# Optimization experiments

Hardware: AMD Instinct MI355X
Metric: run time of the kernel (lower is better)

## Reference

```python
import jax, jax.numpy as jnp
import numpy as np

NUM_GROUPS = 32
EPS = 1e-5


def group_norm(x, gamma, beta):
    b, c, h, w = x.shape
    xg = x.reshape(b, NUM_GROUPS, c // NUM_GROUPS, h, w)
    mu = xg.mean(axis=(2, 3, 4), keepdims=True)
    var = xg.var(axis=(2, 3, 4), keepdims=True)
    xg = (xg - mu) * jax.lax.rsqrt(var + EPS)
    x = xg.reshape(b, c, h, w)
    return x * gamma[None, :, None, None] + beta[None, :, None, None]


def conv1x1(x, w, b):
    # 1x1 conv == per-pixel matmul over channels
    return jnp.einsum('oc,bchw->bohw', w, x) + b[None, :, None, None]


def setup_inputs() -> dict:
    key = jax.random.key(0)
    ks = jax.random.split(key, 6)
    c = 512
    scale = 0.02  # keep logits in a sane range
    return {
        'x': jax.random.normal(ks[0], (2, c, 64, 64), dtype=jnp.float32),
        'gn_w': jnp.ones((c,), jnp.float32),
        'gn_b': jnp.zeros((c,), jnp.float32),
        'wq': jax.random.normal(ks[1], (c, c), jnp.float32) * scale,
        'bq': jnp.zeros((c,), jnp.float32),
        'wk': jax.random.normal(ks[2], (c, c), jnp.float32) * scale,
        'bk': jnp.zeros((c,), jnp.float32),
        'wv': jax.random.normal(ks[3], (c, c), jnp.float32) * scale,
        'bv': jnp.zeros((c,), jnp.float32),
        'wo': jax.random.normal(ks[4], (c, c), jnp.float32) * scale,
        'bo': jnp.zeros((c,), jnp.float32),
    }


def reference(x, gn_w, gn_b, wq, bq, wk, bk, wv, bv, wo, bo):
    b, c, h, w = x.shape
    n = h * w
    h_ = group_norm(x, gn_w, gn_b)
    q = conv1x1(h_, wq, bq).reshape(b, c, n)  # (b,c,n)
    k = conv1x1(h_, wk, bk).reshape(b, c, n)
    v = conv1x1(h_, wv, bv).reshape(b, c, n)
    # scores: (b, n_q, n_k) = q^T k, scaled by c^-0.5
    scores = jnp.einsum('bcq,bck->bqk', q, k) * (c ** -0.5)
    attn = jax.nn.softmax(scores, axis=-1)
    # h_ = v @ attn^T  -> (b, c, n_q)
    out = jnp.einsum('bck,bqk->bcq', v, attn).reshape(b, c, h, w)
    return x + conv1x1(out, wo, bo)
```

## Files before the change

kernel.cpp:

```cpp
#include <hip/hip_runtime.h>

typedef __bf16 bf16_t;
typedef __bf16 bf16x8 __attribute__((ext_vector_type(8)));
typedef __bf16 bf16x4 __attribute__((ext_vector_type(4)));
typedef float  floatx4 __attribute__((ext_vector_type(4)));

#define B_  2
#define C_  512
#define N_  4096
#define EPS 1e-5f
#define SCALE 0.044194173824159216f

__device__ __forceinline__ void gl2lds16(const bf16_t* g, bf16_t* l) {
  __builtin_amdgcn_global_load_lds(
      (const __attribute__((address_space(1))) void*)g,
      (__attribute__((address_space(3))) void*)l, 16, 0, 0);
}

template <int BM, int BN>
__device__ __forceinline__ void gemm_main(
    const bf16_t* __restrict__ A, const bf16_t* __restrict__ B, int K,
    int m0, int n0, floatx4 (&acc)[BM / 32][BN / 32],
    bf16_t* __restrict__ As, bf16_t* __restrict__ Bs) {
  const int tid = threadIdx.x;
  const int w = tid >> 6, l = tid & 63;
  const int wm = (w >> 1) * (BM / 2), wn = (w & 1) * (BN / 2);
  const int lrow = l & 15, lq = l >> 4;
  const int key = lrow & 7;
  const int slot0 = lq ^ key;
  const int slot1 = (4 + lq) ^ key;

  floatx4 zero = {0.f, 0.f, 0.f, 0.f};
#pragma unroll
  for (int mm = 0; mm < BM / 32; mm++)
#pragma unroll
    for (int nn = 0; nn < BN / 32; nn++) acc[mm][nn] = zero;

  for (int k0 = 0; k0 < K; k0 += 64) {
#pragma unroll
    for (int p = 0; p < BM / 32; p++) {
      int gch = p * 256 + tid;
      int r = gch >> 3;
      int cg = (gch & 7) ^ (r & 7);
      gl2lds16(A + (size_t)(m0 + r) * K + k0 + cg * 8, As + gch * 8);
    }
#pragma unroll
    for (int p = 0; p < BN / 32; p++) {
      int gch = p * 256 + tid;
      int r = gch >> 3;
      int cg = (gch & 7) ^ (r & 7);
      gl2lds16(B + (size_t)(n0 + r) * K + k0 + cg * 8, Bs + gch * 8);
    }
    __syncthreads();

    bf16x8 af[BM / 32][2], bfr[BN / 32][2];
#pragma unroll
    for (int mm = 0; mm < BM / 32; mm++) {
      int row = wm + mm * 16 + lrow;
      af[mm][0] = *(const bf16x8*)(As + row * 64 + slot0 * 8);
      af[mm][1] = *(const bf16x8*)(As + row * 64 + slot1 * 8);
    }
#pragma unroll
    for (int nn = 0; nn < BN / 32; nn++) {
      int row = wn + nn * 16 + lrow;
      bfr[nn][0] = *(const bf16x8*)(Bs + row * 64 + slot0 * 8);
      bfr[nn][1] = *(const bf16x8*)(Bs + row * 64 + slot1 * 8);
    }
#pragma unroll
    for (int h = 0; h < 2; h++)
#pragma unroll
      for (int mm = 0; mm < BM / 32; mm++)
#pragma unroll
        for (int nn = 0; nn < BN / 32; nn++)
          acc[mm][nn] = __builtin_amdgcn_mfma_f32_16x16x32_bf16(
              af[mm][h], bfr[nn][h], acc[mm][nn], 0, 0, 0);
    __syncthreads();
  }
}

__global__ __launch_bounds__(256) void gemm_qkv(
    const bf16_t* __restrict__ Wqkv, const bf16_t* __restrict__ h_t,
    bf16_t* __restrict__ q_t, bf16_t* __restrict__ k_t, bf16_t* __restrict__ v,
    const float* __restrict__ bq, const float* __restrict__ bk,
    const float* __restrict__ bv) {
  __shared__ __align__(16) char smem[32768];
  floatx4 acc[4][4];
  const int m0 = blockIdx.y * 128, n0 = blockIdx.x * 128;
  gemm_main<128, 128>(Wqkv, h_t, 512, m0, n0, acc,
                      (bf16_t*)smem, (bf16_t*)(smem + 16384));

  const int tid = threadIdx.x, w = tid >> 6, l = tid & 63;
  const int wm = (w >> 1) * 64, wn = (w & 1) * 64;
  const int lrow = l & 15, q4 = (l >> 4) * 4;
  const int mat = m0 >> 9;
  const float* bias = (mat == 0) ? bq : (mat == 1) ? bk : bv;

  if (mat < 2) {
    bf16_t* ot = (mat == 0) ? q_t : k_t;
#pragma unroll
    for (int mm = 0; mm < 4; mm++) {
#pragma unroll
      for (int nn = 0; nn < 4; nn++) {
        int n = n0 + wn + nn * 16 + lrow;
        int mloc = m0 - mat * 512 + wm + mm * 16 + q4;
        floatx4 a = acc[mm][nn];
        bf16x4 t;
#pragma unroll
        for (int r = 0; r < 4; r++) t[r] = (bf16_t)(a[r] + bias[mloc + r]);
        *(bf16x4*)(ot + (size_t)n * 512 + mloc) = t;
      }
    }
  } else {
    bf16_t* tile = (bf16_t*)smem;
#pragma unroll
    for (int mm = 0; mm < 4; mm++) {
#pragma unroll
      for (int nn = 0; nn < 4; nn++) {
        int colp = wn + nn * 16 + lrow;
        floatx4 a = acc[mm][nn];
#pragma unroll
        for (int r = 0; r < 4; r++) {
          int row = wm + mm * 16 + q4 + r;
          int ch = ((colp >> 3) ^ ((row >> 2) & 15));
          tile[row * 128 + ch * 8 + (colp & 7)] =
              (bf16_t)(a[r] + bias[m0 - 1024 + row]);
        }
      }
    }
    __syncthreads();
    const int bb = n0 >> 12, nl0 = n0 & 4095;
    const int mloc0 = m0 - 1024;
#pragma unroll
    for (int i = 0; i < 8; i++) {
      int c = i * 256 + tid;
      int row = c >> 4, k = c & 15;
      int ch = k ^ ((row >> 2) & 15);
      bf16x8 d = *(const bf16x8*)(tile + row * 128 + ch * 8);
      *(bf16x8*)(v + (size_t)bb * (C_ * N_) + (size_t)(mloc0 + row) * N_ +
                 nl0 + k * 8) = d;
    }
  }
}

__global__ __launch_bounds__(256) void gemm_scores(
    const bf16_t* __restrict__ q_t, const bf16_t* __restrict__ k_t,
    bf16_t* __restrict__ S, size_t sstride, float* __restrict__ L,
    int zbase, int nz) {
  __shared__ __align__(16) char smem[32768];
  const int id = blockIdx.x;
  const int x = id & 7, s = id >> 3;
  const int mi = s & 3, n = (s >> 2) & 31;
  const int zloc = (nz == 2) ? (s >> 7) : 0;
  const int z = (nz == 2) ? zloc : zbase;
  const int m = x * 4 + mi;

  const bf16_t* A = k_t + (size_t)z * (N_ * C_);
  const bf16_t* B = q_t + (size_t)z * (N_ * C_);
  bf16_t* Sb = S + (size_t)zloc * sstride;
  float* Lb = L + (size_t)zloc * N_;
  floatx4 acc[4][4];
  const int m0 = m * 128, n0 = n * 128;
  gemm_main<128, 128>(A, B, 512, m0, n0, acc,
                      (bf16_t*)smem, (bf16_t*)(smem + 16384));

  const int tid = threadIdx.x, w = tid >> 6, l = tid & 63;
  const int wm = (w >> 1) * 64, wn = (w & 1) * 64;
  const int lrow = l & 15, lq = l >> 4, q4 = lq * 4;

  float lsum[4] = {0.f, 0.f, 0.f, 0.f};
#pragma unroll
  for (int mm = 0; mm < 4; mm++) {
#pragma unroll
    for (int nn = 0; nn < 4; nn++) {
      int i  = n0 + wn + nn * 16 + lrow;
      int jb = m0 + wm + mm * 16 + q4;
      floatx4 a = acc[mm][nn];
      float e0 = __expf(a[0] * SCALE);
      float e1 = __expf(a[1] * SCALE);
      float e2 = __expf(a[2] * SCALE);
      float e3 = __expf(a[3] * SCALE);
      lsum[nn] += (e0 + e1) + (e2 + e3);
      bf16x4 t;
      t[0] = (bf16_t)e0; t[1] = (bf16_t)e1;
      t[2] = (bf16_t)e2; t[3] = (bf16_t)e3;
      *(bf16x4*)(Sb + (size_t)i * N_ + jb) = t;
    }
  }
#pragma unroll
  for (int nn = 0; nn < 4; nn++) {
    float vsum = lsum[nn];
    vsum += __shfl_xor(vsum, 16);
    vsum += __shfl_xor(vsum, 32);
    if (lq == 0)
      atomicAdd(Lb + n0 + wn + nn * 16 + lrow, vsum);
  }
}

__global__ __launch_bounds__(512) void gemm_pv(
    const bf16_t* __restrict__ S, size_t sstride, const bf16_t* __restrict__ v,
    const float* __restrict__ L, bf16_t* __restrict__ O_t, int zbase, int nz) {
  __shared__ __align__(16) char smem[49152];
  const int id = blockIdx.x;
  int nb, mb, zloc;
  if (nz == 2) { nb = id >> 6; int g = id & 63; mb = g >> 1; zloc = g & 1; }
  else         { nb = id >> 5; mb = id & 31; zloc = 0; }
  const int z = (nz == 2) ? zloc : zbase;

  const bf16_t* A = S + (size_t)zloc * sstride;
  const bf16_t* B = v + (size_t)z * (C_ * N_);
  const float* Lb = L + (size_t)zloc * N_;
  const int m0 = mb * 128, n0 = nb * 64;

  const int tid = threadIdx.x;
  const int w = tid >> 6, l = tid & 63;
  const int wk = w >> 2;
  const int wl = w & 3;
  const int t2 = tid & 255;
  bf16_t* Ah = (bf16_t*)smem + wk * (128 * 64);
  bf16_t* Bh = (bf16_t*)(smem + 32768) + wk * (64 * 64);

  const int wm = (wl >> 1) * 64, wn = (wl & 1) * 32;
  const int lrow = l & 15, lq = l >> 4;
  const int key = lrow & 7;
  const int slot0 = lq ^ key, slot1 = (4 + lq) ^ key;

  floatx4 acc[4][2];
  floatx4 zero = {0.f, 0.f, 0.f, 0.f};
#pragma unroll
  for (int mm = 0; mm < 4; mm++)
#pragma unroll
    for (int nn = 0; nn < 2; nn++) acc[mm][nn] = zero;

  const int kbase = wk * 2048;
  for (int kk = 0; kk < 2048; kk += 64) {
    const int k0 = kbase + kk;
#pragma unroll
    for (int p = 0; p < 4; p++) {
      int gch = p * 256 + t2;
      int r = gch >> 3;
      int cg = (gch & 7) ^ (r & 7);
      gl2lds16(A + (size_t)(m0 + r) * 4096 + k0 + cg * 8, Ah + gch * 8);
    }
#pragma unroll
    for (int p = 0; p < 2; p++) {
      int gch = p * 256 + t2;
      int r = gch >> 3;
      int cg = (gch & 7) ^ (r & 7);
      gl2lds16(B + (size_t)(n0 + r) * 4096 + k0 + cg * 8, Bh + gch * 8);
    }
    __syncthreads();

    bf16x8 af[4][2], bfr[2][2];
#pragma unroll
    for (int mm = 0; mm < 4; mm++) {
      int row = wm + mm * 16 + lrow;
      af[mm][0] = *(const bf16x8*)(Ah + row * 64 + slot0 * 8);
      af[mm][1] = *(const bf16x8*)(Ah + row * 64 + slot1 * 8);
    }
#pragma unroll
    for (int nn = 0; nn < 2; nn++) {
      int row = wn + nn * 16 + lrow;
      bfr[nn][0] = *(const bf16x8*)(Bh + row * 64 + slot0 * 8);
      bfr[nn][1] = *(const bf16x8*)(Bh + row * 64 + slot1 * 8);
    }
#pragma unroll
    for (int h = 0; h < 2; h++)
#pragma unroll
      for (int mm = 0; mm < 4; mm++)
#pragma unroll
        for (int nn = 0; nn < 2; nn++)
          acc[mm][nn] = __builtin_amdgcn_mfma_f32_16x16x32_bf16(
              af[mm][h], bfr[nn][h], acc[mm][nn], 0, 0, 0);
    __syncthreads();
  }

  floatx4* buf = (floatx4*)smem;
  const int lanebase = wl * 64 + l;
  if (wk == 1) {
#pragma unroll
    for (int mm = 0; mm < 4; mm++)
#pragma unroll
      for (int nn = 0; nn < 2; nn++)
        buf[(mm * 2 + nn) * 256 + lanebase] = acc[mm][nn];
  }
  __syncthreads();

  bf16_t* tile = (bf16_t*)(smem + 32768);
  if (wk == 0) {
    const int q4 = lq * 4;
#pragma unroll
    for (int mm = 0; mm < 4; mm++) {
      const int rowb = wm + mm * 16 + q4;
      float rv0 = 1.0f / Lb[m0 + rowb + 0];
      float rv1 = 1.0f / Lb[m0 + rowb + 1];
      float rv2 = 1.0f / Lb[m0 + rowb + 2];
      float rv3 = 1.0f / Lb[m0 + rowb + 3];
#pragma unroll
      for (int nn = 0; nn < 2; nn++) {
        floatx4 a = acc[mm][nn] + buf[(mm * 2 + nn) * 256 + lanebase];
        a[0] *= rv0; a[1] *= rv1; a[2] *= rv2; a[3] *= rv3;
        int colp = wn + nn * 16 + lrow;
#pragma unroll
        for (int r = 0; r < 4; r++) {
          int row = rowb + r;
          int ch = (colp >> 3) ^ ((row >> 2) & 7);
          tile[row * 64 + ch * 8 + (colp & 7)] = (bf16_t)a[r];
        }
      }
    }
  }
  __syncthreads();
#pragma unroll
  for (int i = 0; i < 2; i++) {
    int c = i * 512 + tid;
    int row = c >> 3, k = c & 7;
    int ch = k ^ ((row >> 2) & 7);
    bf16x8 d = *(const bf16x8*)(tile + row * 64 + ch * 8);
    *(bf16x8*)(O_t + ((size_t)z * N_ + m0 + row) * C_ + n0 + k * 8) = d;
  }
}

__global__ __launch_bounds__(256) void gemm_final(
    const bf16_t* __restrict__ wo, const bf16_t* __restrict__ O_t,
    const float* __restrict__ bo, const float* __restrict__ x,
    float* __restrict__ out) {
  __shared__ __align__(16) char smem[32768];
  floatx4 acc[2][4];
  const int m0 = blockIdx.y * 64, n0 = blockIdx.x * 128;
  gemm_main<64, 128>(wo, O_t, 512, m0, n0, acc,
                     (bf16_t*)smem, (bf16_t*)(smem + 8192));

  const int tid = threadIdx.x, w = tid >> 6, l = tid & 63;
  const int wm = (w >> 1) * 32, wn = (w & 1) * 64;
  const int lrow = l & 15, q4 = (l >> 4) * 4;

  float* tile = (float*)smem;
#pragma unroll
  for (int mm = 0; mm < 2; mm++) {
#pragma unroll
    for (int nn = 0; nn < 4; nn++) {
      int colp = wn + nn * 16 + lrow;
      floatx4 a = acc[mm][nn];
#pragma unroll
      for (int r = 0; r < 4; r++) {
        int row = wm + mm * 16 + q4 + r;
        int ch = (colp >> 2) ^ ((row >> 2) & 31);
        tile[row * 128 + ch * 4 + (colp & 3)] = a[r] + bo[m0 + row];
      }
    }
  }
  __syncthreads();
  const int bb = n0 >> 12, nl0 = n0 & 4095;
#pragma unroll
  for (int i = 0; i < 8; i++) {
    int c = i * 256 + tid;
    int row = c >> 5, k = c & 31;
    int ch = k ^ ((row >> 2) & 31);
    float4 dv = *(const float4*)(tile + row * 128 + ch * 4);
    size_t off = ((size_t)(bb * C_ + m0 + row)) * N_ + nl0 + k * 4;
    float4 xv = *(const float4*)(x + off);
    dv.x += xv.x; dv.y += xv.y; dv.z += xv.z; dv.w += xv.w;
    *(float4*)(out + off) = dv;
  }
}

__global__ __launch_bounds__(256) void prep_kernel(
    const float* __restrict__ s0, const float* __restrict__ s1,
    const float* __restrict__ s2, const float* __restrict__ s3,
    bf16_t* __restrict__ d_qkv, bf16_t* __restrict__ d_o,
    const float* __restrict__ x, float2* __restrict__ part,
    float* __restrict__ L) {
  const int id = blockIdx.x;
  const int tid = threadIdx.x;
  __shared__ float rs[4], rss[4];
  if (id < 4096) {
    int i = id * 256 + tid;
    int mat = i >> 18, idx = i & 262143;
    const float* s = (mat == 0) ? s0 : (mat == 1) ? s1 : (mat == 2) ? s2 : s3;
    if (mat < 3)
      d_qkv[mat * 262144 + idx] = (bf16_t)s[idx];
    else
      d_o[idx] = (bf16_t)s[idx];
  } else if (id < 4608) {
    const int sid = id - 4096;
    const float4* xp = (const float4*)(x + (size_t)sid * 8192);
    float s = 0.f, ss = 0.f;
#pragma unroll
    for (int i = 0; i < 8; i++) {
      float4 v = xp[tid + i * 256];
      s += v.x + v.y + v.z + v.w;
      ss += v.x * v.x + v.y * v.y + v.z * v.z + v.w * v.w;
    }
#pragma unroll
    for (int off = 32; off; off >>= 1) {
      s += __shfl_down(s, off);
      ss += __shfl_down(ss, off);
    }
    if ((tid & 63) == 0) { rs[tid >> 6] = s; rss[tid >> 6] = ss; }
    __syncthreads();
    if (tid == 0) {
      float2 p;
      p.x = rs[0] + rs[1] + rs[2] + rs[3];
      p.y = rss[0] + rss[1] + rss[2] + rss[3];
      part[sid] = p;
    }
  } else {
    float4 z4 = {0.f, 0.f, 0.f, 0.f};
    float4* Lp = (float4*)L;
#pragma unroll
    for (int i = 0; i < 8; i++) Lp[tid + i * 256] = z4;
  }
}

__global__ __launch_bounds__(256) void zeroL_kernel(float* __restrict__ L) {
  float4 z4 = {0.f, 0.f, 0.f, 0.f};
  ((float4*)L)[blockIdx.x * 256 + threadIdx.x] = z4;
}

__global__ __launch_bounds__(256) void gn_apply(
    const float* __restrict__ x, const float* __restrict__ gamma,
    const float* __restrict__ beta, const float2* __restrict__ part,
    bf16_t* __restrict__ h_t) {
  const int id = blockIdx.x;
  const int nc = id & 15, g = (id >> 4) & 31, b = id >> 9;
  const int bg = b * 32 + g;
  float s = 0.f, ss = 0.f;
#pragma unroll
  for (int i = 0; i < 8; i++) {
    float2 p = part[bg * 8 + i];
    s += p.x; ss += p.y;
  }
  const float mean = s * (1.f / 65536.f);
  const float inv = rsqrtf(ss * (1.f / 65536.f) - mean * mean + EPS);

  __shared__ bf16_t tile[256 * 17];
  const int tid = threadIdx.x;
  const int n0 = nc * 256;
#pragma unroll
  for (int i = 0; i < 4; i++) {
    int lin = i * 256 + tid;
    int cl = lin >> 6;
    int n4 = (lin & 63) * 4;
    int c = g * 16 + cl;
    float ga = gamma[c], be = beta[c];
    float4 v = *(const float4*)(x + ((size_t)(b * C_ + c)) * N_ + n0 + n4);
    tile[(n4 + 0) * 17 + cl] = (bf16_t)((v.x - mean) * inv * ga + be);
    tile[(n4 + 1) * 17 + cl] = (bf16_t)((v.y - mean) * inv * ga + be);
    tile[(n4 + 2) * 17 + cl] = (bf16_t)((v.z - mean) * inv * ga + be);
    tile[(n4 + 3) * 17 + cl] = (bf16_t)((v.w - mean) * inv * ga + be);
  }
  __syncthreads();
  union { bf16_t h[8]; uint4 u; } p0, p1;
#pragma unroll
  for (int c = 0; c < 8; c++)  p0.h[c] = tile[tid * 17 + c];
#pragma unroll
  for (int c = 0; c < 8; c++)  p1.h[c] = tile[tid * 17 + 8 + c];
  bf16_t* dst = h_t + ((size_t)(b * N_ + n0 + tid)) * C_ + g * 16;
  *(uint4*)dst = p0.u;
  *(uint4*)(dst + 8) = p1.u;
}

extern "C" void kernel_launch(void* const* d_in, const int* in_sizes, int n_in,
                              void* d_out, int out_size, void* d_ws, size_t ws_size,
                              hipStream_t stream) {
  const float* x    = (const float*)d_in[0];
  const float* gn_w = (const float*)d_in[1];
  const float* gn_b = (const float*)d_in[2];
  const float* wq   = (const float*)d_in[3];
  const float* bq   = (const float*)d_in[4];
  const float* wk   = (const float*)d_in[5];
  const float* bk   = (const float*)d_in[6];
  const float* wv   = (const float*)d_in[7];
  const float* bv   = (const float*)d_in[8];
  const float* wo   = (const float*)d_in[9];
  const float* bo   = (const float*)d_in[10];
  float* out = (float*)d_out;

  char* ws = (char*)d_ws;
  bf16_t* h_t  = (bf16_t*)(ws);
  bf16_t* q_t  = (bf16_t*)(ws + (8u << 20));
  bf16_t* k_t  = (bf16_t*)(ws + (16u << 20));
  bf16_t* v_   = (bf16_t*)(ws + (24u << 20));
  bf16_t* O_t  = (bf16_t*)(ws + (32u << 20));
  bf16_t* wqkv = (bf16_t*)(ws + (40u << 20));
  bf16_t* wob  = (bf16_t*)(ws + (42u << 20));
  float2* gnp  = (float2*)(ws + (43u << 20));
  float*  L    = (float*)(ws + (43u << 20) + 8192);
  bf16_t* S    = (bf16_t*)(ws + (44u << 20));

  const size_t SN = (size_t)N_ * N_;
  const int nz = (ws_size >= (44u << 20) + 2 * SN * sizeof(bf16_t)) ? 2 : 1;

  prep_kernel<<<4609, 256, 0, stream>>>(wq, wk, wv, wo, wqkv, wob, x, gnp, L);
  gn_apply<<<1024, 256, 0, stream>>>(x, gn_w, gn_b, gnp, h_t);

  gemm_qkv<<<dim3(64, 12), 256, 0, stream>>>(wqkv, h_t, q_t, k_t, v_,
                                             bq, bk, bv);

  if (nz == 2) {
    gemm_scores<<<2048, 256, 0, stream>>>(q_t, k_t, S, SN, L, 0, 2);
    gemm_pv<<<512, 512, 0, stream>>>(S, SN, v_, L, O_t, 0, 2);
  } else {
    for (int b = 0; b < B_; b++) {
      zeroL_kernel<<<4, 256, 0, stream>>>(L);
      gemm_scores<<<1024, 256, 0, stream>>>(q_t, k_t, S, 0, L, b, 1);
      gemm_pv<<<256, 512, 0, stream>>>(S, 0, v_, L, O_t, b, 1);
    }
  }

  gemm_final<<<dim3(64, 8), 256, 0, stream>>>(wob, O_t, bo, x, out);
}
```

Before: 223.5 us.

## Split K across two wave groups in scores GEMM with LDS reduction

The scores GEMM now runs 512 threads per block. The two halves of the block each compute half of the 512-long K reduction into separate LDS buffers, then one half adds its partial accumulators into the other through shared memory before the exp/store epilogue. The goal is more waves per tile to hide load latency, and the inner loop is written inline with swizzled direct-to-LDS loads instead of calling gemm_main. In exchange, LDS per block doubles to 64KB, an extra reduction pass goes through LDS, and half the waves sit idle during the epilogue.

New measurement: 227.9 us. About the same (+2.0%).

```diff
diff --git a/kernel.cpp b/kernel.cpp
--- a/kernel.cpp
+++ b/kernel.cpp
@@ -142,11 +142,11 @@
   }
 }
 
-__global__ __launch_bounds__(256) void gemm_scores(
+__global__ __launch_bounds__(512) void gemm_scores(
     const bf16_t* __restrict__ q_t, const bf16_t* __restrict__ k_t,
     bf16_t* __restrict__ S, size_t sstride, float* __restrict__ L,
     int zbase, int nz) {
-  __shared__ __align__(16) char smem[32768];
+  __shared__ __align__(16) char smem[65536];
   const int id = blockIdx.x;
   const int x = id & 7, s = id >> 3;
   const int mi = s & 3, n = (s >> 2) & 31;
@@ -158,41 +158,111 @@
   const bf16_t* B = q_t + (size_t)z * (N_ * C_);
   bf16_t* Sb = S + (size_t)zloc * sstride;
   float* Lb = L + (size_t)zloc * N_;
+  const int m0 = m * 128, n0 = n * 128;
+
+  const int tid = threadIdx.x;
+  const int w = tid >> 6, l = tid & 63;
+  const int wk = w >> 2;
+  const int wl = w & 3;
+  const int t2 = tid & 255;
+  bf16_t* Ah = (bf16_t*)smem + wk * (128 * 64);
+  bf16_t* Bh = (bf16_t*)(smem + 32768) + wk * (128 * 64);
+
+  const int wm = (wl >> 1) * 64, wn = (wl & 1) * 64;
+  const int lrow = l & 15, lq = l >> 4;
+  const int key = lrow & 7;
+  const int slot0 = lq ^ key, slot1 = (4 + lq) ^ key;
+
   floatx4 acc[4][4];
-  const int m0 = m * 128, n0 = n * 128;
-  gemm_main<128, 128>(A, B, 512, m0, n0, acc,
-                      (bf16_t*)smem, (bf16_t*)(smem + 16384));
-
-  const int tid = threadIdx.x, w = tid >> 6, l = tid & 63;
-  const int wm = (w >> 1) * 64, wn = (w & 1) * 64;
-  const int lrow = l & 15, lq = l >> 4, q4 = lq * 4;
-
-  float lsum[4] = {0.f, 0.f, 0.f, 0.f};
-#pragma unroll
-  for (int mm = 0; mm < 4; mm++) {
+  floatx4 zero = {0.f, 0.f, 0.f, 0.f};
+#pragma unroll
+  for (int mm = 0; mm < 4; mm++)
+#pragma unroll
+    for (int nn = 0; nn < 4; nn++) acc[mm][nn] = zero;
+
+  const int kbase = wk * 256;
+  for (int kk = 0; kk < 256; kk += 64) {
+    const int k0 = kbase + kk;
+#pragma unroll
+    for (int p = 0; p < 4; p++) {
+      int gch = p * 256 + t2;
+      int r = gch >> 3;
+      int cg = (gch & 7) ^ (r & 7);
+      gl2lds16(A + (size_t)(m0 + r) * C_ + k0 + cg * 8, Ah + gch * 8);
+    }
+#pragma unroll
+    for (int p = 0; p < 4; p++) {
+      int gch = p * 256 + t2;
+      int r = gch >> 3;
+      int cg = (gch & 7) ^ (r & 7);
+      gl2lds16(B + (size_t)(n0 + r) * C_ + k0 + cg * 8, Bh + gch * 8);
+    }
+    __syncthreads();
+
+    bf16x8 af[4][2], bfr[4][2];
+#pragma unroll
+    for (int mm = 0; mm < 4; mm++) {
+      int row = wm + mm * 16 + lrow;
+      af[mm][0] = *(const bf16x8*)(Ah + row * 64 + slot0 * 8);
+      af[mm][1] = *(const bf16x8*)(Ah + row * 64 + slot1 * 8);
+    }
 #pragma unroll
     for (int nn = 0; nn < 4; nn++) {
-      int i  = n0 + wn + nn * 16 + lrow;
-      int jb = m0 + wm + mm * 16 + q4;
-      floatx4 a = acc[mm][nn];
-      float e0 = __expf(a[0] * SCALE);
-      float e1 = __expf(a[1] * SCALE);
-      float e2 = __expf(a[2] * SCALE);
-      float e3 = __expf(a[3] * SCALE);
-      lsum[nn] += (e0 + e1) + (e2 + e3);
-      bf16x4 t;
-      t[0] = (bf16_t)e0; t[1] = (bf16_t)e1;
-      t[2] = (bf16_t)e2; t[3] = (bf16_t)e3;
-      *(bf16x4*)(Sb + (size_t)i * N_ + jb) = t;
-    }
-  }
-#pragma unroll
-  for (int nn = 0; nn < 4; nn++) {
-    float vsum = lsum[nn];
-    vsum += __shfl_xor(vsum, 16);
-    vsum += __shfl_xor(vsum, 32);
-    if (lq == 0)
-      atomicAdd(Lb + n0 + wn + nn * 16 + lrow, vsum);
+      int row = wn + nn * 16 + lrow;
+      bfr[nn][0] = *(const bf16x8*)(Bh + row * 64 + slot0 * 8);
+      bfr[nn][1] = *(const bf16x8*)(Bh + row * 64 + slot1 * 8);
+    }
+#pragma unroll
+    for (int h = 0; h < 2; h++)
+#pragma unroll
+      for (int mm = 0; mm < 4; mm++)
+#pragma unroll
+        for (int nn = 0; nn < 4; nn++)
+          acc[mm][nn] = __builtin_amdgcn_mfma_f32_16x16x32_bf16(
+              af[mm][h], bfr[nn][h], acc[mm][nn], 0, 0, 0);
+    __syncthreads();
+  }
+
+  floatx4* buf = (floatx4*)smem;
+  const int lanebase = wl * 64 + l;
+  if (wk == 1) {
+#pragma unroll
+    for (int mm = 0; mm < 4; mm++)
+#pragma unroll
+      for (int nn = 0; nn < 4; nn++)
+        buf[(mm * 4 + nn) * 256 + lanebase] = acc[mm][nn];
+  }
+  __syncthreads();
+
+  if (wk == 0) {
+    const int q4 = lq * 4;
+    float lsum[4] = {0.f, 0.f, 0.f, 0.f};
+#pragma unroll
+    for (int mm = 0; mm < 4; mm++) {
+#pragma unroll
+      for (int nn = 0; nn < 4; nn++) {
+        floatx4 a = acc[mm][nn] + buf[(mm * 4 + nn) * 256 + lanebase];
+        int i  = n0 + wn + nn * 16 + lrow;
+        int jb = m0 + wm + mm * 16 + q4;
+        float e0 = __expf(a[0] * SCALE);
+        float e1 = __expf(a[1] * SCALE);
+        float e2 = __expf(a[2] * SCALE);
+        float e3 = __expf(a[3] * SCALE);
+        lsum[nn] += (e0 + e1) + (e2 + e3);
+        bf16x4 t;
+        t[0] = (bf16_t)e0; t[1] = (bf16_t)e1;
+        t[2] = (bf16_t)e2; t[3] = (bf16_t)e3;
+        *(bf16x4*)(Sb + (size_t)i * N_ + jb) = t;
+      }
+    }
+#pragma unroll
+    for (int nn = 0; nn < 4; nn++) {
+      float vsum = lsum[nn];
+      vsum += __shfl_xor(vsum, 16);
+      vsum += __shfl_xor(vsum, 32);
+      if (lq == 0)
+        atomicAdd(Lb + n0 + wn + nn * 16 + lrow, vsum);
+    }
   }
 }
 
@@ -498,12 +568,12 @@
                                              bq, bk, bv);
 
   if (nz == 2) {
-    gemm_scores<<<2048, 256, 0, stream>>>(q_t, k_t, S, SN, L, 0, 2);
+    gemm_scores<<<2048, 512, 0, stream>>>(q_t, k_t, S, SN, L, 0, 2);
     gemm_pv<<<512, 512, 0, stream>>>(S, SN, v_, L, O_t, 0, 2);
   } else {
     for (int b = 0; b < B_; b++) {
       zeroL_kernel<<<4, 256, 0, stream>>>(L);
-      gemm_scores<<<1024, 256, 0, stream>>>(q_t, k_t, S, 0, L, b, 1);
+      gemm_scores<<<1024, 512, 0, stream>>>(q_t, k_t, S, 0, L, b, 1);
       gemm_pv<<<256, 512, 0, stream>>>(S, 0, v_, L, O_t, b, 1);
     }
   }
```

## Store attention probabilities and V in FP8 and use FP8 MFMA for PV

Applied to the files above, without the earlier changes.

The unnormalized exp scores matrix S and the V tensor are now written in FP8 (e4m3) instead of bf16, and the PV GEMM loads FP8 tiles and uses the 16x16x32 fp8 MFMA. This halves the bytes for the large N×N score matrix written by the scores kernel and read by the PV kernel, and doubles MFMA throughput per tile. LDS layout and swizzles are rewritten for byte-sized elements. It risks accuracy loss from FP8 rounding of the probabilities and V values.

After: 230.6 us. +3.2%, slower.

```diff
diff --git a/kernel.cpp b/kernel.cpp
--- a/kernel.cpp
+++ b/kernel.cpp
@@ -11,10 +11,14 @@
 #define EPS 1e-5f
 #define SCALE 0.044194173824159216f
 
-__device__ __forceinline__ void gl2lds16(const bf16_t* g, bf16_t* l) {
+__device__ __forceinline__ void gl2lds16(const void* g, void* l) {
   __builtin_amdgcn_global_load_lds(
       (const __attribute__((address_space(1))) void*)g,
       (__attribute__((address_space(3))) void*)l, 16, 0, 0);
+}
+
+__device__ __forceinline__ unsigned char f8(float x) {
+  return (unsigned char)(__builtin_amdgcn_cvt_pk_fp8_f32(x, x, 0, false) & 0xff);
 }
 
 template <int BM, int BN>
@@ -80,7 +84,8 @@
 
 __global__ __launch_bounds__(256) void gemm_qkv(
     const bf16_t* __restrict__ Wqkv, const bf16_t* __restrict__ h_t,
-    bf16_t* __restrict__ q_t, bf16_t* __restrict__ k_t, bf16_t* __restrict__ v,
+    bf16_t* __restrict__ q_t, bf16_t* __restrict__ k_t,
+    unsigned char* __restrict__ v8,
     const float* __restrict__ bq, const float* __restrict__ bk,
     const float* __restrict__ bv) {
   __shared__ __align__(16) char smem[32768];
@@ -111,7 +116,7 @@
       }
     }
   } else {
-    bf16_t* tile = (bf16_t*)smem;
+    unsigned char* tile8 = (unsigned char*)smem;
 #pragma unroll
     for (int mm = 0; mm < 4; mm++) {
 #pragma unroll
@@ -121,9 +126,9 @@
 #pragma unroll
         for (int r = 0; r < 4; r++) {
           int row = wm + mm * 16 + q4 + r;
-          int ch = ((colp >> 3) ^ ((row >> 2) & 15));
-          tile[row * 128 + ch * 8 + (colp & 7)] =
-              (bf16_t)(a[r] + bias[m0 - 1024 + row]);
+          int ch = (colp >> 4) ^ ((row >> 2) & 7);
+          tile8[row * 128 + ch * 16 + (colp & 15)] =
+              f8(a[r] + bias[m0 - 1024 + row]);
         }
       }
     }
@@ -131,20 +136,20 @@
     const int bb = n0 >> 12, nl0 = n0 & 4095;
     const int mloc0 = m0 - 1024;
 #pragma unroll
-    for (int i = 0; i < 8; i++) {
+    for (int i = 0; i < 4; i++) {
       int c = i * 256 + tid;
-      int row = c >> 4, k = c & 15;
-      int ch = k ^ ((row >> 2) & 15);
-      bf16x8 d = *(const bf16x8*)(tile + row * 128 + ch * 8);
-      *(bf16x8*)(v + (size_t)bb * (C_ * N_) + (size_t)(mloc0 + row) * N_ +
-                 nl0 + k * 8) = d;
+      int row = c >> 3, k = c & 7;
+      int ch = k ^ ((row >> 2) & 7);
+      uint4 d = *(const uint4*)(tile8 + row * 128 + ch * 16);
+      *(uint4*)(v8 + (size_t)bb * (C_ * N_) + (size_t)(mloc0 + row) * N_ +
+                nl0 + k * 16) = d;
     }
   }
 }
 
 __global__ __launch_bounds__(256) void gemm_scores(
     const bf16_t* __restrict__ q_t, const bf16_t* __restrict__ k_t,
-    bf16_t* __restrict__ S, size_t sstride, float* __restrict__ L,
+    unsigned char* __restrict__ S8, size_t sstride, float* __restrict__ L,
     int zbase, int nz) {
   __shared__ __align__(16) char smem[32768];
   const int id = blockIdx.x;
@@ -156,7 +161,7 @@
 
   const bf16_t* A = k_t + (size_t)z * (N_ * C_);
   const bf16_t* B = q_t + (size_t)z * (N_ * C_);
-  bf16_t* Sb = S + (size_t)zloc * sstride;
+  unsigned char* Sb = S8 + (size_t)zloc * sstride;
   float* Lb = L + (size_t)zloc * N_;
   floatx4 acc[4][4];
   const int m0 = m * 128, n0 = n * 128;
@@ -165,7 +170,7 @@
 
   const int tid = threadIdx.x, w = tid >> 6, l = tid & 63;
   const int wm = (w >> 1) * 64, wn = (w & 1) * 64;
-  const int lrow = l & 15, lq = l >> 4, q4 = lq * 4;
+  const int lrow = l & 15, lq = l >> 4;
 
   float lsum[4] = {0.f, 0.f, 0.f, 0.f};
 #pragma unroll
@@ -173,17 +178,16 @@
 #pragma unroll
     for (int nn = 0; nn < 4; nn++) {
       int i  = n0 + wn + nn * 16 + lrow;
-      int jb = m0 + wm + mm * 16 + q4;
+      int jb = m0 + wm + mm * 16 + lq * 4;
       floatx4 a = acc[mm][nn];
       float e0 = __expf(a[0] * SCALE);
       float e1 = __expf(a[1] * SCALE);
       float e2 = __expf(a[2] * SCALE);
       float e3 = __expf(a[3] * SCALE);
       lsum[nn] += (e0 + e1) + (e2 + e3);
-      bf16x4 t;
-      t[0] = (bf16_t)e0; t[1] = (bf16_t)e1;
-      t[2] = (bf16_t)e2; t[3] = (bf16_t)e3;
-      *(bf16x4*)(Sb + (size_t)i * N_ + jb) = t;
+      unsigned int p = __builtin_amdgcn_cvt_pk_fp8_f32(e0, e1, 0, false);
+      p = __builtin_amdgcn_cvt_pk_fp8_f32(e2, e3, p, true);
+      *(unsigned int*)(Sb + (size_t)i * N_ + jb) = p;
     }
   }
 #pragma unroll
@@ -197,8 +201,9 @@
 }
 
 __global__ __launch_bounds__(512) void gemm_pv(
-    const bf16_t* __restrict__ S, size_t sstride, const bf16_t* __restrict__ v,
-    const float* __restrict__ L, bf16_t* __restrict__ O_t, int zbase, int nz) {
+    const unsigned char* __restrict__ S8, size_t sstride,
+    const unsigned char* __restrict__ v8, const float* __restrict__ L,
+    bf16_t* __restrict__ O_t, int zbase, int nz) {
   __shared__ __align__(16) char smem[49152];
   const int id = blockIdx.x;
   int nb, mb, zloc;
@@ -206,8 +211,8 @@
   else         { nb = id >> 5; mb = id & 31; zloc = 0; }
   const int z = (nz == 2) ? zloc : zbase;
 
-  const bf16_t* A = S + (size_t)zloc * sstride;
-  const bf16_t* B = v + (size_t)z * (C_ * N_);
+  const unsigned char* A = S8 + (size_t)zloc * sstride;
+  const unsigned char* B = v8 + (size_t)z * (C_ * N_);
   const float* Lb = L + (size_t)zloc * N_;
   const int m0 = mb * 128, n0 = nb * 64;
 
@@ -216,13 +221,14 @@
   const int wk = w >> 2;
   const int wl = w & 3;
   const int t2 = tid & 255;
-  bf16_t* Ah = (bf16_t*)smem + wk * (128 * 64);
-  bf16_t* Bh = (bf16_t*)(smem + 32768) + wk * (64 * 64);
+  unsigned char* Ah = (unsigned char*)smem + wk * (128 * 64);
+  unsigned char* Bh = (unsigned char*)(smem + 16384) + wk * (64 * 64);
 
   const int wm = (wl >> 1) * 64, wn = (wl & 1) * 32;
   const int lrow = l & 15, lq = l >> 4;
-  const int key = lrow & 7;
-  const int slot0 = lq ^ key, slot1 = (4 + lq) ^ key;
+  const int key4 = lrow & 3;
+  const int fo0 = (((lq >> 1) + 0) ^ key4) * 16 + (lq & 1) * 8;
+  const int fo1 = (((lq >> 1) + 2) ^ key4) * 16 + (lq & 1) * 8;
 
   floatx4 acc[4][2];
   floatx4 zero = {0.f, 0.f, 0.f, 0.f};
@@ -235,33 +241,32 @@
   for (int kk = 0; kk < 2048; kk += 64) {
     const int k0 = kbase + kk;
 #pragma unroll
-    for (int p = 0; p < 4; p++) {
-      int gch = p * 256 + t2;
-      int r = gch >> 3;
-      int cg = (gch & 7) ^ (r & 7);
-      gl2lds16(A + (size_t)(m0 + r) * 4096 + k0 + cg * 8, Ah + gch * 8);
-    }
-#pragma unroll
     for (int p = 0; p < 2; p++) {
       int gch = p * 256 + t2;
-      int r = gch >> 3;
-      int cg = (gch & 7) ^ (r & 7);
-      gl2lds16(B + (size_t)(n0 + r) * 4096 + k0 + cg * 8, Bh + gch * 8);
+      int r = gch >> 2;
+      int cg = (gch & 3) ^ (r & 3);
+      gl2lds16(A + (size_t)(m0 + r) * 4096 + k0 + cg * 16, Ah + gch * 16);
+    }
+    {
+      int gch = t2;
+      int r = gch >> 2;
+      int cg = (gch & 3) ^ (r & 3);
+      gl2lds16(B + (size_t)(n0 + r) * 4096 + k0 + cg * 16, Bh + gch * 16);
     }
     __syncthreads();
 
-    bf16x8 af[4][2], bfr[2][2];
+    long af[4][2], bfr[2][2];
 #pragma unroll
     for (int mm = 0; mm < 4; mm++) {
       int row = wm + mm * 16 + lrow;
-      af[mm][0] = *(const bf16x8*)(Ah + row * 64 + slot0 * 8);
-      af[mm][1] = *(const bf16x8*)(Ah + row * 64 + slot1 * 8);
+      af[mm][0] = *(const long*)(Ah + row * 64 + fo0);
+      af[mm][1] = *(const long*)(Ah + row * 64 + fo1);
     }
 #pragma unroll
     for (int nn = 0; nn < 2; nn++) {
       int row = wn + nn * 16 + lrow;
-      bfr[nn][0] = *(const bf16x8*)(Bh + row * 64 + slot0 * 8);
-      bfr[nn][1] = *(const bf16x8*)(Bh + row * 64 + slot1 * 8);
+      bfr[nn][0] = *(const long*)(Bh + row * 64 + fo0);
+      bfr[nn][1] = *(const long*)(Bh + row * 64 + fo1);
     }
 #pragma unroll
     for (int h = 0; h < 2; h++)
@@ -269,7 +274,7 @@
       for (int mm = 0; mm < 4; mm++)
 #pragma unroll
         for (int nn = 0; nn < 2; nn++)
-          acc[mm][nn] = __builtin_amdgcn_mfma_f32_16x16x32_bf16(
+          acc[mm][nn] = __builtin_amdgcn_mfma_f32_16x16x32_fp8_fp8(
               af[mm][h], bfr[nn][h], acc[mm][nn], 0, 0, 0);
     __syncthreads();
   }
@@ -480,31 +485,31 @@
   bf16_t* h_t  = (bf16_t*)(ws);
   bf16_t* q_t  = (bf16_t*)(ws + (8u << 20));
   bf16_t* k_t  = (bf16_t*)(ws + (16u << 20));
-  bf16_t* v_   = (bf16_t*)(ws + (24u << 20));
+  unsigned char* v8 = (unsigned char*)(ws + (24u << 20));
   bf16_t* O_t  = (bf16_t*)(ws + (32u << 20));
   bf16_t* wqkv = (bf16_t*)(ws + (40u << 20));
   bf16_t* wob  = (bf16_t*)(ws + (42u << 20));
   float2* gnp  = (float2*)(ws + (43u << 20));
   float*  L    = (float*)(ws + (43u << 20) + 8192);
-  bf16_t* S    = (bf16_t*)(ws + (44u << 20));
+  unsigned char* S8 = (unsigned char*)(ws + (44u << 20));
 
   const size_t SN = (size_t)N_ * N_;
-  const int nz = (ws_size >= (44u << 20) + 2 * SN * sizeof(bf16_t)) ? 2 : 1;
+  const int nz = (ws_size >= (44u << 20) + 2 * SN) ? 2 : 1;
 
   prep_kernel<<<4609, 256, 0, stream>>>(wq, wk, wv, wo, wqkv, wob, x, gnp, L);
   gn_apply<<<1024, 256, 0, stream>>>(x, gn_w, gn_b, gnp, h_t);
 
-  gemm_qkv<<<dim3(64, 12), 256, 0, stream>>>(wqkv, h_t, q_t, k_t, v_,
+  gemm_qkv<<<dim3(64, 12), 256, 0, stream>>>(wqkv, h_t, q_t, k_t, v8,
                                              bq, bk, bv);
 
   if (nz == 2) {
-    gemm_scores<<<2048, 256, 0, stream>>>(q_t, k_t, S, SN, L, 0, 2);
-    gemm_pv<<<512, 512, 0, stream>>>(S, SN, v_, L, O_t, 0, 2);
+    gemm_scores<<<2048, 256, 0, stream>>>(q_t, k_t, S8, SN, L, 0, 2);
+    gemm_pv<<<512, 512, 0, stream>>>(S8, SN, v8, L, O_t, 0, 2);
   } else {
     for (int b = 0; b < B_; b++) {
       zeroL_kernel<<<4, 256, 0, stream>>>(L);
-      gemm_scores<<<1024, 256, 0, stream>>>(q_t, k_t, S, 0, L, b, 1);
-      gemm_pv<<<256, 512, 0, stream>>>(S, 0, v_, L, O_t, b, 1);
+      gemm_scores<<<1024, 256, 0, stream>>>(q_t, k_t, S8, 0, L, b, 1);
+      gemm_pv<<<256, 512, 0, stream>>>(S8, 0, v8, L, O_t, b, 1);
     }
   }
 
```
